# Performance work log

Hardware: AMD Instinct MI355X
Metric: run time of the kernel (lower is better)

Reference implementation:

```python
import jax, jax.numpy as jnp
import numpy as np
from jax import lax

HEADS = 8
AGENT = 49            # agent_num
POOL = 7              # int(sqrt(agent_num))
DOWN_H, DOWN_W = 7, 7  # downstream_agent_shape
DIM = 256
WIN = 56              # sqrt(num_patches)


def _resize(x, oh, ow):
    # torch F.interpolate(mode='bilinear', align_corners=False) equivalent for upsample/identity
    return jax.image.resize(x, x.shape[:-2] + (oh, ow), method='bilinear', antialias=False)


def _bias_pipeline(bias, H, W):
    # bias: (heads, AGENT, h0, w0) -> (heads, H*W, DOWN_H*DOWN_W)
    h = bias.shape[0]
    pb = _resize(bias, H, W)                                     # (h, 49, H, W)
    pb = pb.reshape(h, POOL, POOL, H * W).transpose(0, 3, 1, 2)  # (h, HW, 7, 7)
    pb = _resize(pb, DOWN_H, DOWN_W)                             # (h, HW, 7, 7)
    return pb.reshape(h, H * W, DOWN_H * DOWN_W)


def setup_inputs() -> dict:
    key = jax.random.key(0)
    ks = jax.random.split(key, 16)
    b, H, W = 16, WIN, WIN
    n, c, h = H * W, DIM, HEADS
    s = 0.02
    f32 = jnp.float32
    return {
        "x": jax.random.normal(ks[0], (b, n, c), f32),
        "H": H,
        "W": W,
        "Wq": jax.random.normal(ks[1], (c, c), f32) * c ** -0.5,
        "Wkv": jax.random.normal(ks[2], (2 * c, c), f32) * c ** -0.5,
        "Wproj": jax.random.normal(ks[3], (c, c), f32) * c ** -0.5,
        "bproj": jnp.zeros((c,), f32),
        "dwc_w": jax.random.normal(ks[4], (c, 1, 3, 3), f32) * 0.1,
        "dwc_b": jnp.zeros((c,), f32),
        "an_bias": jax.random.normal(ks[5], (h, AGENT, 7, 7), f32) * s,
        "na_bias": jax.random.normal(ks[6], (h, AGENT, 7, 7), f32) * s,
        "ah_bias": jax.random.normal(ks[7], (1, h, AGENT, WIN, 1), f32) * s,
        "aw_bias": jax.random.normal(ks[8], (1, h, AGENT, 1, WIN), f32) * s,
        "ha_bias": jax.random.normal(ks[9], (1, h, WIN, 1, AGENT), f32) * s,
        "wa_bias": jax.random.normal(ks[10], (1, h, 1, WIN, AGENT), f32) * s,
    }


def reference(x, H, W, Wq, Wkv, Wproj, bproj, dwc_w, dwc_b,
              an_bias, na_bias, ah_bias, aw_bias, ha_bias, wa_bias):
    b, n, c = x.shape
    h = HEADS
    hd = c // h
    T = n // 2
    scale = hd ** -0.5
    dan = DOWN_H * DOWN_W

    q_lin = x @ Wq.T                       # (b,n,c)
    kv = x @ Wkv.T                         # (b,n,2c)
    k_lin, v_lin = kv[..., :c], kv[..., c:]

    # adaptive avg pool of q to (7,7) agent grid (H, W divisible by 7)
    qg = q_lin.reshape(b, DOWN_H, H // DOWN_H, DOWN_W, W // DOWN_W, c).mean(axis=(2, 4))
    agent = qg.reshape(b, dan, h, hd).transpose(0, 2, 1, 3)   # (b,h,49,hd)

    q = q_lin.reshape(b, n, h, hd).transpose(0, 2, 1, 3)      # (b,h,n,hd)
    k = k_lin.reshape(b, n, h, hd).transpose(0, 2, 1, 3)
    v = v_lin.reshape(b, n, h, hd).transpose(0, 2, 1, 3)

    # agent -> kv attention biases
    pb1 = _bias_pipeline(an_bias, H, W).transpose(0, 2, 1)    # (h,49,HW)
    pb2 = _bias_pipeline((ah_bias + aw_bias)[0], H, W).transpose(0, 2, 1)
    position_bias = (pb1 + pb2)[None]                         # (1,h,49,HW)

    agent_attn = jax.nn.softmax(
        jnp.einsum('bhad,bhnd->bhan', agent * scale, k) + position_bias, axis=-1)
    agent_v = jnp.einsum('bhan,bhnd->bhad', agent_attn, v)    # (b,h,49,hd)

    # query -> agent attention biases
    ab1 = _bias_pipeline(na_bias, H, W)                       # (h,HW,49)
    ab2 = _bias_pipeline((ha_bias + wa_bias)[0].transpose(0, 3, 1, 2), H, W)
    agent_bias = (ab1 + ab2)[None]                            # (1,h,HW,49)

    # top-T query selection, then bilinear upsample of scores back to n rows
    token_w = jax.nn.softmax(q.mean(axis=-1), axis=-1)        # (b,h,n)
    _, top_idx = lax.top_k(token_w, T)                        # (b,h,T)
    q_top = jnp.take_along_axis(q, top_idx[..., None], axis=2)  # (b,h,T,hd)
    q2 = jnp.einsum('bhtd,bhad->bhta', q_top, agent)          # (b,h,T,49)
    q2 = _resize(q2, n, dan) * scale                          # (b,h,n,49)

    q_attn = jax.nn.softmax(q2 + agent_bias, axis=-1)
    out = jnp.einsum('bhna,bhad->bhnd', q_attn, agent_v)
    out = out.transpose(0, 2, 1, 3).reshape(b, n, c)

    # depthwise conv branch on v
    v_img = v.transpose(0, 2, 1, 3).reshape(b, H, W, c).transpose(0, 3, 1, 2)  # (b,c,H,W)
    dw = lax.conv_general_dilated(v_img, dwc_w, (1, 1), ((1, 1), (1, 1)),
                                  feature_group_count=c)
    dw = dw + dwc_b[None, :, None, None]
    out = out + dw.transpose(0, 2, 3, 1).reshape(b, n, c)
    return out @ Wproj.T + bproj
```

## Files before the change

kernel.cpp:

```cpp
#include <hip/hip_runtime.h>
#include <stdint.h>

typedef _Float16 f16;
typedef _Float16 half8 __attribute__((ext_vector_type(8)));
typedef float f32x4 __attribute__((ext_vector_type(4)));

#define NBATCH 16
#define NTOK 3136
#define NTOT 50176
#define NH 8
#define NA 49
#define NAP 64
#define TTOP 1568
#define NTILES 196
#define PBH 200704
#define SCALE 0.17677669529663687f

__device__ __forceinline__ f32x4 mfma16(half8 a, half8 b, f32x4 c) {
  return __builtin_amdgcn_mfma_f32_16x16x32_f16(a, b, c, 0, 0, 0);
}

__device__ __forceinline__ void gload16(const void* g, void* l) {
  __builtin_amdgcn_global_load_lds(
      (const __attribute__((address_space(1))) void*)g,
      (__attribute__((address_space(3))) void*)l, 16, 0, 0);
}

__global__ __launch_bounds__(256) void k_prep_w(const float* Wq, const float* Wkv, const float* Wproj,
                                                f16* wqkv, f16* wproj) {
  int total1 = 768 * 256;
  int total = total1 + 256 * 256;
  for (int i = blockIdx.x * 256 + threadIdx.x; i < total; i += gridDim.x * 256) {
    if (i < total1) {
      int j = i >> 8, k = i & 255;
      float v = (j < 256) ? Wq[j * 256 + k] : Wkv[(j - 256) * 256 + k];
      wqkv[i] = (f16)v;
    } else {
      int i2 = i - total1;
      wproj[i2] = (f16)Wproj[i2];
    }
  }
}

__global__ __launch_bounds__(256) void k_cvt_x(const float* x, f16* xh, long total) {
  long i = (long)blockIdx.x * blockDim.x + threadIdx.x;
  long stride = (long)gridDim.x * blockDim.x;
  for (long e = i * 8; e < total; e += stride * 8) {
    float4 v0 = *(const float4*)(x + e);
    float4 v1 = *(const float4*)(x + e + 4);
    half8 o = {(f16)v0.x, (f16)v0.y, (f16)v0.z, (f16)v0.w,
               (f16)v1.x, (f16)v1.y, (f16)v1.z, (f16)v1.w};
    *(half8*)(xh + e) = o;
  }
}

__global__ __launch_bounds__(256) void k_bias(const float* an_b, const float* na_b,
                                              const float* ah_b, const float* aw_b,
                                              const float* ha_b, const float* wa_b,
                                              float* pos_bias, float* agent_bias) {
  int n = blockIdx.x * 256 + threadIdx.x;
  int h = blockIdx.y;
  if (n >= NTOK) return;
  int y = n / 56, x = n - y * 56;
  float py = (y + 0.5f) * 0.125f - 0.5f;
  float px = (x + 0.5f) * 0.125f - 0.5f;
  int iy0 = (int)floorf(py); float fy = py - (float)iy0;
  int ix0 = (int)floorf(px); float fx = px - (float)ix0;
  int y0 = max(iy0, 0), y1 = min(iy0 + 1, 6);
  int x0 = max(ix0, 0), x1 = min(ix0 + 1, 6);
  float w00 = (1.f - fy) * (1.f - fx), w01 = (1.f - fy) * fx;
  float w10 = fy * (1.f - fx), w11 = fy * fx;
  for (int a = 0; a < NA; ++a) {
    const float* pa = an_b + (h * NA + a) * 49;
    float up_an = w00 * pa[y0 * 7 + x0] + w01 * pa[y0 * 7 + x1] +
                  w10 * pa[y1 * 7 + x0] + w11 * pa[y1 * 7 + x1];
    const float* pn = na_b + (h * NA + a) * 49;
    float up_na = w00 * pn[y0 * 7 + x0] + w01 * pn[y0 * 7 + x1] +
                  w10 * pn[y1 * 7 + x0] + w11 * pn[y1 * 7 + x1];
    float pb = up_an + ah_b[(h * NA + a) * 56 + y] + aw_b[(h * NA + a) * 56 + x];
    pos_bias[((size_t)(h * NAP + a)) * NTOK + n] = pb;
    float ab = up_na + ha_b[(h * 56 + y) * NA + a] + wa_b[(h * 56 + x) * NA + a];
    agent_bias[((size_t)(h * NAP + a)) * NTOK + n] = ab;
  }
  for (int a = NA; a < NAP; ++a)
    pos_bias[((size_t)(h * NAP + a)) * NTOK + n] = 0.f;
}

template <bool PROJ>
__global__ __launch_bounds__(256) void k_gemm(const f16* __restrict__ A, const f16* __restrict__ Bw,
                                              f16* __restrict__ CH, float* __restrict__ Cf32,
                                              const float* __restrict__ bias, int N) {
  __shared__ __align__(16) char lds[16384];
  int per = gridDim.x >> 3;
  int wrk = (blockIdx.x & 7) * per + (blockIdx.x >> 3);
  int nNT = N >> 7;
  int mt = wrk / nNT, nt = wrk - mt * nNT;
  int m0 = mt * 128, n0 = nt * 128;
  int tid = threadIdx.x, w = tid >> 6, l = tid & 63, lr = l & 15, lg = l >> 4;
  int wm = w >> 1, wn = w & 1;
  f32x4 acc[4][4] = {};
  const char* Bb = (const char*)Bw + (size_t)n0 * 512;
  int rowA0 = 32 * w + (l >> 2);
  int rowA1 = rowA0 + 16;
  int koff = (l & 3) * 16;
  char* ldsA0 = lds + (2 * w) * 1024;
  char* ldsA1 = lds + (2 * w + 1) * 1024;
  char* ldsB0 = lds + 8192 + (2 * w) * 1024;
  char* ldsB1 = lds + 8192 + (2 * w + 1) * 1024;

  for (int k0 = 0; k0 < 256; k0 += 32) {
    if (PROJ) {
      const char* Ab = (const char*)A + ((size_t)(k0 >> 5) * NTOT + m0) * 64;
      gload16(Ab + (size_t)rowA0 * 64 + koff, ldsA0);
      gload16(Ab + (size_t)rowA1 * 64 + koff, ldsA1);
    } else {
      const char* Ab = (const char*)A + (size_t)m0 * 512 + k0 * 2;
      gload16(Ab + (size_t)rowA0 * 512 + koff, ldsA0);
      gload16(Ab + (size_t)rowA1 * 512 + koff, ldsA1);
    }
    gload16(Bb + (size_t)rowA0 * 512 + k0 * 2 + koff, ldsB0);
    gload16(Bb + (size_t)rowA1 * 512 + k0 * 2 + koff, ldsB1);
    __syncthreads();
    half8 af[4], bf[4];
#pragma unroll
    for (int m4 = 0; m4 < 4; ++m4) {
      int row = wm * 64 + m4 * 16 + lr;
      af[m4] = *(const half8*)(lds + row * 64 + lg * 16);
    }
#pragma unroll
    for (int n4 = 0; n4 < 4; ++n4) {
      int row = wn * 64 + n4 * 16 + lr;
      bf[n4] = *(const half8*)(lds + 8192 + row * 64 + lg * 16);
    }
#pragma unroll
    for (int m4 = 0; m4 < 4; ++m4)
#pragma unroll
      for (int n4 = 0; n4 < 4; ++n4)
        acc[m4][n4] = mfma16(af[m4], bf[n4], acc[m4][n4]);
    __syncthreads();
  }

#pragma unroll
  for (int n4 = 0; n4 < 4; ++n4) {
    int n = n0 + wn * 64 + n4 * 16 + lr;
    f16* bp = PROJ ? nullptr : (CH + (size_t)(n >> 5) * NTOT * 32 + (n & 31));
#pragma unroll
    for (int m4 = 0; m4 < 4; ++m4)
#pragma unroll
      for (int r = 0; r < 4; ++r) {
        int m = m0 + wm * 64 + m4 * 16 + lg * 4 + r;
        if (PROJ)
          Cf32[(size_t)m * N + n] = acc[m4][n4][r] + bias[n];
        else
          bp[(size_t)m * 32] = (f16)acc[m4][n4][r];
      }
  }
}

__global__ __launch_bounds__(256) void k_pool_tw(const f16* qkvH, f16* agent, float* tw) {
  int bh = blockIdx.x, b = bh >> 3, h = bh & 7;
  int tid = threadIdx.x;
  const f16* qp0 = qkvH + ((size_t)h * NTOT + (size_t)b * NTOK) * 32;
  {
    int a = tid >> 2, c = tid & 3;
    float s8[8] = {};
    if (a < NA) {
      int dh = a / 7, dwi = a - dh * 7;
      for (int i = 0; i < 8; ++i)
#pragma unroll
        for (int j = 0; j < 8; ++j) {
          int tok = (dh * 8 + i) * 56 + dwi * 8 + j;
          half8 v = *(const half8*)(qp0 + (size_t)tok * 32 + c * 8);
#pragma unroll
          for (int e = 0; e < 8; ++e) s8[e] += (float)v[e];
        }
    }
    half8 o;
#pragma unroll
    for (int e = 0; e < 8; ++e) o[e] = (f16)(s8[e] * (SCALE / 64.f));
    *(half8*)(agent + (size_t)bh * NAP * 32 + a * 32 + c * 8) = o;
  }
  for (int n = tid; n < NTOK; n += 256) {
    const half8* qp = (const half8*)(qp0 + (size_t)n * 32);
    float sum = 0.f;
#pragma unroll
    for (int j = 0; j < 4; ++j) {
      half8 v = qp[j];
#pragma unroll
      for (int e = 0; e < 8; ++e) sum += (float)v[e];
    }
    tw[(size_t)bh * NTOK + n] = sum * (1.f / 32.f);
  }
}

template <int J>
__device__ __forceinline__ void stage_local(unsigned long long (&key)[16], int kmask, int base) {
#pragma unroll
  for (int e = 0; e < 16; ++e) {
    if ((e & J) == 0) {
      bool desc = (((base + e) & kmask) == 0);
      unsigned long long a = key[e], c = key[e | J];
      if ((a < c) == desc) { key[e] = c; key[e | J] = a; }
    }
  }
}

__global__ __launch_bounds__(256, 1) void k_topk(const float* tw, int* topidx) {
  __shared__ unsigned long long lk[4096 + 256];
  int bh = blockIdx.x, tid = threadIdx.x;
  const float* p = tw + (size_t)bh * NTOK;
  unsigned long long key[16];
  int base = tid * 16;
#pragma unroll
  for (int e = 0; e < 16; ++e) {
    int s = base + e;
    float v = (s < NTOK) ? p[s] : -1e30f;
    unsigned ub = __float_as_uint(v);
    ub = (ub & 0x80000000u) ? ~ub : (ub | 0x80000000u);
    unsigned low = (s < NTOK) ? ~(unsigned)s : 0u;
    key[e] = ((unsigned long long)ub << 32) | low;
  }
  stage_local<1>(key, 2, base);
  stage_local<2>(key, 4, base);  stage_local<1>(key, 4, base);
  stage_local<4>(key, 8, base);  stage_local<2>(key, 8, base);  stage_local<1>(key, 8, base);
  stage_local<8>(key, 16, base); stage_local<4>(key, 16, base);
  stage_local<2>(key, 16, base); stage_local<1>(key, 16, base);
  for (int k = 32; k <= 4096; k <<= 1) {
    bool desc = ((base & k) == 0);
    for (int j = k >> 1; j >= 16; j >>= 1) {
      int m = j >> 4;
      bool takeMax = (((tid & m) == 0) == desc);
      unsigned long long pv[16];
      if (m <= 32) {
#pragma unroll
        for (int e = 0; e < 16; ++e) pv[e] = __shfl_xor(key[e], m, 64);
      } else {
        __syncthreads();
#pragma unroll
        for (int e = 0; e < 16; ++e) { int ix = base + e; lk[ix + (ix >> 4)] = key[e]; }
        __syncthreads();
        int pb = (tid ^ m) * 16;
#pragma unroll
        for (int e = 0; e < 16; ++e) { int ix = pb + e; pv[e] = lk[ix + (ix >> 4)]; }
      }
#pragma unroll
      for (int e = 0; e < 16; ++e)
        key[e] = takeMax ? (key[e] > pv[e] ? key[e] : pv[e])
                         : (key[e] < pv[e] ? key[e] : pv[e]);
    }
    stage_local<8>(key, k, base);
    stage_local<4>(key, k, base);
    stage_local<2>(key, k, base);
    stage_local<1>(key, k, base);
  }
  if (tid < TTOP / 16) {
    int* op = topidx + (size_t)bh * TTOP + base;
#pragma unroll
    for (int e = 0; e < 16; ++e) op[e] = (int)(~(unsigned)key[e]);
  }
}

__global__ __launch_bounds__(256) void k_vt(const f16* qkvH, f16* vt) {
  __shared__ __align__(16) f16 t[64][40];
  int bh = blockIdx.y, b = bh >> 3, h = bh & 7;
  int n0 = blockIdx.x * 64;
  int tid = threadIdx.x;
  const f16* vp = qkvH + ((size_t)(16 + h) * NTOT + (size_t)b * NTOK + n0) * 32;
  {
    int nl = tid >> 2, c = tid & 3;
    *(half8*)(&t[nl][c * 8]) = *(const half8*)(vp + (size_t)nl * 32 + c * 8);
  }
  __syncthreads();
  for (int s = tid; s < 64 * 32; s += 256) {
    int d = s >> 6, nl = s & 63;
    vt[((size_t)(bh * 32 + d)) * NTOK + n0 + nl] = t[nl][d];
  }
}

__global__ __launch_bounds__(256) void k_flash(const f16* qkvH, const f16* agent, const f16* vt,
                                               const float* pos_bias, float* agent_v) {
  __shared__ __align__(16) f16 pbuf[4][64][40];
  __shared__ float ored[64][33];
  __shared__ float rssum[64];
  int bh = blockIdx.x, b = bh >> 3, h = bh & 7;
  int tid = threadIdx.x, w = tid >> 6, l = tid & 63, lr = l & 15, lg = l >> 4;
  half8 afrag[4];
#pragma unroll
  for (int mt = 0; mt < 4; ++mt)
    afrag[mt] = *(const half8*)(agent + ((size_t)bh * 64 + mt * 16 + lr) * 32 + lg * 8);
  f32x4 o[4][2] = {};
  float rs[4][4] = {};
  const f16* kbase = qkvH + ((size_t)(8 + h) * NTOT + (size_t)b * NTOK) * 32;
  const f16* vtb = vt + (size_t)bh * 32 * NTOK;
  const float* pbb = pos_bias + (size_t)h * NAP * NTOK;
  f32x4 zero = {};
  for (int n0 = w * 32; n0 < NTOK; n0 += 128) {
#pragma unroll
    for (int t2 = 0; t2 < 2; ++t2) {
      int nc = n0 + t2 * 16;
      half8 kf = *(const half8*)(kbase + (size_t)(nc + lr) * 32 + lg * 8);
#pragma unroll
      for (int mt = 0; mt < 4; ++mt) {
        f32x4 s = mfma16(afrag[mt], kf, zero);
#pragma unroll
        for (int r = 0; r < 4; ++r) {
          int a = mt * 16 + lg * 4 + r;
          float pv = __expf(s[r] + pbb[(size_t)a * NTOK + nc + lr]);
          rs[mt][r] += pv;
          pbuf[w][a][t2 * 16 + lr] = (f16)pv;
        }
      }
    }
    half8 pf[4];
#pragma unroll
    for (int mt = 0; mt < 4; ++mt)
      pf[mt] = *(const half8*)(&pbuf[w][mt * 16 + lr][lg * 8]);
#pragma unroll
    for (int dt = 0; dt < 2; ++dt) {
      half8 vf = *(const half8*)(vtb + (size_t)(dt * 16 + lr) * NTOK + n0 + lg * 8);
#pragma unroll
      for (int mt = 0; mt < 4; ++mt)
        o[mt][dt] = mfma16(pf[mt], vf, o[mt][dt]);
    }
  }
#pragma unroll
  for (int mt = 0; mt < 4; ++mt)
#pragma unroll
    for (int r = 0; r < 4; ++r) {
      float v = rs[mt][r];
      for (int off = 1; off < 16; off <<= 1) v += __shfl_xor(v, off, 64);
      rs[mt][r] = v;
    }
  for (int s = tid; s < 64 * 33; s += 256) ((float*)ored)[s] = 0.f;
  if (tid < 64) rssum[tid] = 0.f;
  __syncthreads();
  for (int ww = 0; ww < 4; ++ww) {
    if (w == ww) {
      if (lr == 0)
#pragma unroll
        for (int mt = 0; mt < 4; ++mt)
#pragma unroll
          for (int r = 0; r < 4; ++r) rssum[mt * 16 + lg * 4 + r] += rs[mt][r];
#pragma unroll
      for (int mt = 0; mt < 4; ++mt)
#pragma unroll
        for (int dt = 0; dt < 2; ++dt)
#pragma unroll
          for (int r = 0; r < 4; ++r)
            ored[mt * 16 + lg * 4 + r][dt * 16 + lr] += o[mt][dt][r];
    }
    __syncthreads();
  }
  for (int s = tid; s < NA * 32; s += 256) {
    int a = s >> 5, d = s & 31;
    agent_v[(size_t)bh * NA * 32 + s] = ored[a][d] / rssum[a];
  }
}

__global__ __launch_bounds__(256) void k_psm(const f16* qkvH, const f16* agent, const int* topidx,
                                             const float* agent_bias, f16* P) {
  __shared__ __align__(16) f16 q2buf[144][88];
  int chunk = blockIdx.x, bh = blockIdx.y, b = bh >> 3, h = bh & 7;
  int tid = threadIdx.x, w = tid >> 6, l = tid & 63, lr = l & 15, lg = l >> 4;
  const f16* qplane = qkvH + ((size_t)h * NTOT + (size_t)b * NTOK) * 32;
  half8 bfrag[4];
#pragma unroll
  for (int nt = 0; nt < 4; ++nt)
    bfrag[nt] = *(const half8*)(agent + ((size_t)bh * 64 + nt * 16 + lr) * 32 + lg * 8);
  int jbase = chunk * 128 - 8;
  f32x4 zero = {};
  for (int mt = w; mt < 9; mt += 4) {
    int j = jbase + mt * 16 + lr;
    int jc = min(max(j, 0), TTOP - 1);
    int tok = topidx[(size_t)bh * TTOP + jc];
    half8 qf = *(const half8*)(qplane + (size_t)tok * 32 + lg * 8);
#pragma unroll
    for (int nt = 0; nt < 4; ++nt) {
      f32x4 s = mfma16(qf, bfrag[nt], zero);
#pragma unroll
      for (int r = 0; r < 4; ++r)
        q2buf[mt * 16 + lg * 4 + r][nt * 16 + lr] = (f16)s[r];
    }
  }
  __syncthreads();
  int g = chunk * 256 + tid;
  if (g >= NTOK) return;
  int hi = g >> 1;
  int jA, jB; float wAq, wBq;
  if (g & 1) { jA = hi; jB = hi + 1; wAq = 0.75f; wBq = 0.25f; }
  else       { jA = hi - 1; jB = hi; wAq = 0.25f; wBq = 0.75f; }
  jA = min(max(jA, 0), TTOP - 1);
  jB = min(max(jB, 0), TTOP - 1);
  int lA = jA - jbase, lB = jB - jbase;
  const float* ab = agent_bias + (size_t)h * NAP * NTOK + g;
  f16* Pb = P + (size_t)bh * PBH;
  int tile = g >> 4, lrr = g & 15;
  float ssum = 0.f;
  half8 oo[7];
#pragma unroll
  for (int c = 0; c < 7; ++c) {
    half8 a8 = *(const half8*)(&q2buf[lA][c * 8]);
    half8 b8 = *(const half8*)(&q2buf[lB][c * 8]);
#pragma unroll
    for (int e = 0; e < 8; ++e) {
      int a = c * 8 + e;
      float pv = 0.f;
      if (a < NA) {
        float v = wAq * (float)a8[e] + wBq * (float)b8[e] + ab[(size_t)a * NTOK];
        pv = __expf(v);
        ssum += pv;
      }
      oo[c][e] = (f16)pv;
    }
  }
  f16 invs = (f16)(1.f / ssum);
  half8 iv8 = {invs, invs, invs, invs, invs, invs, invs, invs};
#pragma unroll
  for (int c = 0; c < 7; ++c)
    *(half8*)(Pb + ((size_t)(tile * 8 + c) * 16 + lrr) * 8) = oo[c] * iv8;
  half8 z = {};
  *(half8*)(Pb + ((size_t)(tile * 8 + 7) * 16 + lrr) * 8) = z;
}

__global__ __launch_bounds__(256) void k_out(const f16* __restrict__ P,
                                             const float* __restrict__ agent_v,
                                             const f16* __restrict__ qkvH,
                                             const float* __restrict__ dwc_w,
                                             const float* __restrict__ dwc_b,
                                             f16* __restrict__ preH) {
  __shared__ __align__(16) f16 avT[32][72];
  __shared__ __align__(16) f16 ctile[224][40];
  __shared__ float wconv[9][32];
  __shared__ float bconv[32];
  int chunk = blockIdx.x, bh = blockIdx.y, b = bh >> 3, h = bh & 7;
  int tid = threadIdx.x, w = tid >> 6, l = tid & 63, lr = l & 15, lg = l >> 4;
  int y0 = chunk * 4;
  const f16* vp = qkvH + ((size_t)(16 + h) * NTOT + (size_t)b * NTOK) * 32;
  const f16* Pb = P + (size_t)bh * PBH;
  half8 pa0[4], pa1[4];
#pragma unroll
  for (int i = 0; i < 4; ++i) {
    int lt = w * 4 + i;
    if (lt < 14) {
      const f16* Pt = Pb + (size_t)(chunk * 14 + lt) * 1024;
      pa0[i] = *(const half8*)(Pt + ((size_t)(0 + lg) * 16 + lr) * 8);
      pa1[i] = *(const half8*)(Pt + ((size_t)(4 + lg) * 16 + lr) * 8);
    }
  }
  for (int s = tid; s < 32 * 64; s += 256) {
    int d = s >> 6, a = s & 63;
    avT[d][a] = (a < NA) ? (f16)agent_v[((size_t)bh * NA + a) * 32 + d] : (f16)0.f;
  }
  for (int s = tid; s < 32 * 9; s += 256) {
    int d = s / 9, t = s - d * 9;
    wconv[t][d] = dwc_w[(size_t)(h * 32 + d) * 9 + t];
  }
  if (tid < 32) bconv[tid] = dwc_b[h * 32 + tid];
  __syncthreads();
  half8 bf[2][2];
#pragma unroll
  for (int nt = 0; nt < 2; ++nt)
#pragma unroll
    for (int ks = 0; ks < 2; ++ks)
      bf[nt][ks] = *(const half8*)(&avT[0][0] + (size_t)(nt * 16 + lr) * 72 + ks * 32 + lg * 8);
#pragma unroll
  for (int i = 0; i < 4; ++i) {
    int lt = w * 4 + i;
    if (lt >= 14) continue;
    f32x4 acc0 = {}, acc1 = {};
    acc0 = mfma16(pa0[i], bf[0][0], acc0);
    acc0 = mfma16(pa1[i], bf[0][1], acc0);
    acc1 = mfma16(pa0[i], bf[1][0], acc1);
    acc1 = mfma16(pa1[i], bf[1][1], acc1);
    int ltrow = lt * 16 + lg * 4;
#pragma unroll
    for (int r = 0; r < 4; ++r) {
      ctile[ltrow + r][lr] = (f16)acc0[r];
      ctile[ltrow + r][16 + lr] = (f16)acc1[r];
    }
  }
  __syncthreads();
  if (tid >= 224) return;
  int g = chunk * 224 + tid;
  int ly = tid / 56, x = tid - ly * 56;
  int y = y0 + ly;
  float accd[32];
#pragma unroll
  for (int c = 0; c < 4; ++c) {
    half8 cv = *(const half8*)(&ctile[tid][c * 8]);
#pragma unroll
    for (int e = 0; e < 8; ++e) accd[c * 8 + e] = (float)cv[e] + bconv[c * 8 + e];
  }
#pragma unroll
  for (int ky = 0; ky < 3; ++ky) {
    int gy = y + ky - 1;
    if (gy < 0 || gy >= 56) continue;
#pragma unroll
    for (int kx = 0; kx < 3; ++kx) {
      int xx = x + kx - 1;
      if (xx < 0 || xx >= 56) continue;
      int t = ky * 3 + kx;
      const f16* vt9 = vp + (size_t)(gy * 56 + xx) * 32;
#pragma unroll
      for (int c = 0; c < 4; ++c) {
        half8 vv = *(const half8*)(vt9 + c * 8);
#pragma unroll
        for (int e = 0; e < 8; ++e) accd[c * 8 + e] += wconv[t][c * 8 + e] * (float)vv[e];
      }
    }
  }
  f16* op = preH + ((size_t)h * NTOT + (size_t)b * NTOK + g) * 32;
#pragma unroll
  for (int c = 0; c < 4; ++c) {
    half8 o;
#pragma unroll
    for (int e = 0; e < 8; ++e) o[e] = (f16)accd[c * 8 + e];
    *(half8*)(op + c * 8) = o;
  }
}

extern "C" void kernel_launch(void* const* d_in, const int* in_sizes, int n_in,
                              void* d_out, int out_size, void* d_ws, size_t ws_size,
                              hipStream_t stream) {
  const float* x     = (const float*)d_in[0];
  const float* Wq    = (const float*)d_in[3];
  const float* Wkv   = (const float*)d_in[4];
  const float* Wproj = (const float*)d_in[5];
  const float* bproj = (const float*)d_in[6];
  const float* dwc_w = (const float*)d_in[7];
  const float* dwc_b = (const float*)d_in[8];
  const float* an_b  = (const float*)d_in[9];
  const float* na_b  = (const float*)d_in[10];
  const float* ah_b  = (const float*)d_in[11];
  const float* aw_b  = (const float*)d_in[12];
  const float* ha_b  = (const float*)d_in[13];
  const float* wa_b  = (const float*)d_in[14];

  char* ws = (char*)d_ws;
  size_t off = 0;
  auto alloc = [&](size_t bytes) {
    void* p = ws + off;
    off = (off + bytes + 255) & ~(size_t)255;
    return p;
  };
  f16* wqkv    = (f16*)alloc((size_t)768 * 256 * 2);
  f16* wproj   = (f16*)alloc((size_t)256 * 256 * 2);
  f16* qkvH    = (f16*)alloc((size_t)24 * NTOT * 32 * 2);
  float* posb  = (float*)alloc((size_t)8 * NAP * NTOK * 4);
  float* agb   = (float*)alloc((size_t)8 * NAP * NTOK * 4);
  f16* agent   = (f16*)alloc((size_t)128 * NAP * 32 * 2);
  float* tw    = (float*)alloc((size_t)128 * NTOK * 4);
  int* topidx  = (int*)alloc((size_t)128 * TTOP * 4);
  f16* vt      = (f16*)alloc((size_t)128 * 32 * NTOK * 2);
  float* agv   = (float*)alloc((size_t)128 * NA * 32 * 4);
  f16* preH    = (f16*)alloc((size_t)8 * NTOT * 32 * 2);
  f16* P       = (f16*)alloc((size_t)128 * PBH * 2);
  f16* xh      = P;

  k_prep_w<<<1024, 256, 0, stream>>>(Wq, Wkv, Wproj, wqkv, wproj);
  k_cvt_x<<<2048, 256, 0, stream>>>(x, xh, (long)NTOT * 256);
  k_bias<<<dim3(13, 8), 256, 0, stream>>>(an_b, na_b, ah_b, aw_b, ha_b, wa_b, posb, agb);
  k_gemm<false><<<2352, 256, 0, stream>>>(xh, wqkv, qkvH, nullptr, nullptr, 768);
  k_pool_tw<<<128, 256, 0, stream>>>(qkvH, agent, tw);
  k_topk<<<128, 256, 0, stream>>>(tw, topidx);
  k_vt<<<dim3(49, 128), 256, 0, stream>>>(qkvH, vt);
  k_flash<<<128, 256, 0, stream>>>(qkvH, agent, vt, posb, agv);
  k_psm<<<dim3(13, 128), 256, 0, stream>>>(qkvH, agent, topidx, agb, P);
  k_out<<<dim3(14, 128), 256, 0, stream>>>(P, agv, qkvH, dwc_w, dwc_b, preH);
  k_gemm<true><<<784, 256, 0, stream>>>(preH, wproj, nullptr, (float*)d_out, bproj, 256);
}
```

Before: 258.0 us.

## Split flash agent-attention over token parts and stage QKV GEMM epilogue through LDS

The agent-attention kernel used to run only 128 blocks, one per batch-head, on a GPU with many more CUs. It now splits the token range into four parts, writes partial outputs and row sums, and adds a small reduction kernel that combines them and normalizes. Separately, the QKV GEMM epilogue now stages the f16 tile in LDS, so the head-split layout is written with 16-byte vector stores instead of scattered 2-byte stores. The cost is an extra launch, a partial-result round trip through global memory, and extra barriers in the GEMM epilogue.

```diff
diff --git a/kernel.cpp b/kernel.cpp
--- a/kernel.cpp
+++ b/kernel.cpp
@@ -15,6 +15,7 @@
 #define NTILES 196
 #define PBH 200704
 #define SCALE 0.17677669529663687f
+#define FPARTS 4
 
 __device__ __forceinline__ f32x4 mfma16(half8 a, half8 b, f32x4 c) {
   return __builtin_amdgcn_mfma_f32_16x16x32_f16(a, b, c, 0, 0, 0);
@@ -140,20 +141,41 @@
     __syncthreads();
   }
 
-#pragma unroll
-  for (int n4 = 0; n4 < 4; ++n4) {
-    int n = n0 + wn * 64 + n4 * 16 + lr;
-    f16* bp = PROJ ? nullptr : (CH + (size_t)(n >> 5) * NTOT * 32 + (n & 31));
-#pragma unroll
-    for (int m4 = 0; m4 < 4; ++m4)
-#pragma unroll
-      for (int r = 0; r < 4; ++r) {
-        int m = m0 + wm * 64 + m4 * 16 + lg * 4 + r;
-        if (PROJ)
+  if (PROJ) {
+#pragma unroll
+    for (int n4 = 0; n4 < 4; ++n4) {
+      int n = n0 + wn * 64 + n4 * 16 + lr;
+#pragma unroll
+      for (int m4 = 0; m4 < 4; ++m4)
+#pragma unroll
+        for (int r = 0; r < 4; ++r) {
+          int m = m0 + wm * 64 + m4 * 16 + lg * 4 + r;
           Cf32[(size_t)m * N + n] = acc[m4][n4][r] + bias[n];
-        else
-          bp[(size_t)m * 32] = (f16)acc[m4][n4][r];
+        }
+    }
+  } else {
+    f16* cl = (f16*)lds;
+    int rr = tid >> 2, c4 = tid & 3;
+#pragma unroll
+    for (int hm = 0; hm < 2; ++hm) {
+      __syncthreads();
+      if (wm == hm) {
+#pragma unroll
+        for (int m4 = 0; m4 < 4; ++m4)
+#pragma unroll
+          for (int n4 = 0; n4 < 4; ++n4)
+#pragma unroll
+            for (int r = 0; r < 4; ++r)
+              cl[(m4 * 16 + lg * 4 + r) * 128 + wn * 64 + n4 * 16 + lr] = (f16)acc[m4][n4][r];
       }
+      __syncthreads();
+#pragma unroll
+      for (int cc = 0; cc < 4; ++cc) {
+        int pn = (n0 >> 5) + cc;
+        half8 v = *(const half8*)(cl + rr * 128 + cc * 32 + c4 * 8);
+        *(half8*)(CH + ((size_t)pn * NTOT + m0 + hm * 64 + rr) * 32 + c4 * 8) = v;
+      }
+    }
   }
 }
 
@@ -278,11 +300,11 @@
 }
 
 __global__ __launch_bounds__(256) void k_flash(const f16* qkvH, const f16* agent, const f16* vt,
-                                               const float* pos_bias, float* agent_v) {
+                                               const float* pos_bias, float* opart, float* rspart) {
   __shared__ __align__(16) f16 pbuf[4][64][40];
   __shared__ float ored[64][33];
   __shared__ float rssum[64];
-  int bh = blockIdx.x, b = bh >> 3, h = bh & 7;
+  int part = blockIdx.x, bh = blockIdx.y, b = bh >> 3, h = bh & 7;
   int tid = threadIdx.x, w = tid >> 6, l = tid & 63, lr = l & 15, lg = l >> 4;
   half8 afrag[4];
 #pragma unroll
@@ -294,7 +316,7 @@
   const f16* vtb = vt + (size_t)bh * 32 * NTOK;
   const float* pbb = pos_bias + (size_t)h * NAP * NTOK;
   f32x4 zero = {};
-  for (int n0 = w * 32; n0 < NTOK; n0 += 128) {
+  for (int n0 = (part * 4 + w) * 32; n0 < NTOK; n0 += 512) {
 #pragma unroll
     for (int t2 = 0; t2 < 2; ++t2) {
       int nc = n0 + t2 * 16;
@@ -351,9 +373,26 @@
     }
     __syncthreads();
   }
+  int pp = bh * FPARTS + part;
   for (int s = tid; s < NA * 32; s += 256) {
     int a = s >> 5, d = s & 31;
-    agent_v[(size_t)bh * NA * 32 + s] = ored[a][d] / rssum[a];
+    opart[((size_t)pp * 64 + a) * 32 + d] = ored[a][d];
+  }
+  if (tid < NA) rspart[(size_t)pp * 64 + tid] = rssum[tid];
+}
+
+__global__ __launch_bounds__(256) void k_fred(const float* opart, const float* rspart, float* agv) {
+  int bh = blockIdx.x, tid = threadIdx.x;
+  for (int s = tid; s < NA * 32; s += 256) {
+    int a = s >> 5, d = s & 31;
+    float o = 0.f, rs = 0.f;
+#pragma unroll
+    for (int p = 0; p < FPARTS; ++p) {
+      int pp = bh * FPARTS + p;
+      o += opart[((size_t)pp * 64 + a) * 32 + d];
+      rs += rspart[(size_t)pp * 64 + a];
+    }
+    agv[(size_t)bh * NA * 32 + s] = o / rs;
   }
 }
 
@@ -553,6 +592,8 @@
   int* topidx  = (int*)alloc((size_t)128 * TTOP * 4);
   f16* vt      = (f16*)alloc((size_t)128 * 32 * NTOK * 2);
   float* agv   = (float*)alloc((size_t)128 * NA * 32 * 4);
+  float* opart = (float*)alloc((size_t)128 * FPARTS * 64 * 32 * 4);
+  float* rspart= (float*)alloc((size_t)128 * FPARTS * 64 * 4);
   f16* preH    = (f16*)alloc((size_t)8 * NTOT * 32 * 2);
   f16* P       = (f16*)alloc((size_t)128 * PBH * 2);
   f16* xh      = P;
@@ -564,7 +605,8 @@
   k_pool_tw<<<128, 256, 0, stream>>>(qkvH, agent, tw);
   k_topk<<<128, 256, 0, stream>>>(tw, topidx);
   k_vt<<<dim3(49, 128), 256, 0, stream>>>(qkvH, vt);
-  k_flash<<<128, 256, 0, stream>>>(qkvH, agent, vt, posb, agv);
+  k_flash<<<dim3(FPARTS, 128), 256, 0, stream>>>(qkvH, agent, vt, posb, opart, rspart);
+  k_fred<<<128, 256, 0, stream>>>(opart, rspart, agv);
   k_psm<<<dim3(13, 128), 256, 0, stream>>>(qkvH, agent, topidx, agb, P);
   k_out<<<dim3(14, 128), 256, 0, stream>>>(P, agv, qkvH, dwc_w, dwc_b, preH);
   k_gemm<true><<<784, 256, 0, stream>>>(preH, wproj, nullptr, (float*)d_out, bproj, 256);
```

New measurement: 245.6 us. 4.8% less time.
